# Kernel tuning notes

Measured on AMD Instinct MI355X. Metric: run time of the kernel, lower is better.

The kernel has to match this reference:

```python
import jax, jax.numpy as jnp
import numpy as np

M, P, B = 64, 256, 4096  # blocks per row/col, block size, batch


def setup_inputs() -> dict:
    key = jax.random.key(0)
    ks = jax.random.split(key, 6)
    u = lambda k, shape: jax.random.uniform(k, shape, jnp.float32, -0.1, 0.1)
    return {
        "x": jax.random.normal(ks[0], (B, M * P), dtype=jnp.float32),
        "Wd": u(ks[1], (M, P, P)),      # diag blocks (nn.Linear weights)
        "Wu": u(ks[2], (M - 1, P, P)),  # upper off-diagonal blocks
        "Wl": u(ks[3], (M - 1, P, P)),  # lower off-diagonal blocks
        "Wtr": u(ks[4], (P, P)),        # top-right corner block (periodic)
        "Wbl": u(ks[5], (P, P)),        # bottom-left corner block (periodic)
    }


def reference(x, Wd, Wu, Wl, Wtr, Wbl):
    # BlockXDiag forward, diag_type='tri', periodic=True, transpose=False,
    # bias=False, activation=None (identity). nn.Linear: o = x @ W.T
    Bsz = x.shape[0]
    xb = x.reshape(Bsz, M, P)  # [B, M, P]
    # diagonal: result[:, i] = x_i @ Wd[i].T  -> batched over all M blocks
    out = jnp.einsum('bip,iqp->biq', xb, Wd)
    # upper band: result[:, i] += x_{i+1} @ Wu[i].T, i in [0, M-2]
    out = out.at[:, : M - 1].add(jnp.einsum('bip,iqp->biq', xb[:, 1:], Wu))
    # lower band: result[:, i] += x_{i-1} @ Wl[i-1].T, i in [1, M-1]
    out = out.at[:, 1:].add(jnp.einsum('bip,iqp->biq', xb[:, : M - 1], Wl))
    # periodic corners
    out = out.at[:, 0].add(xb[:, M - 1] @ Wtr.T)
    out = out.at[:, M - 1].add(xb[:, 0] @ Wbl.T)
    return out.reshape(Bsz, M * P)
```

## Files before the change

kernel.cpp:

```cpp
#include <hip/hip_runtime.h>


#define MB   64
#define PB   256
#define NPR  16384
#define BSZ  4096
#define BM   128
#define BN   128
#define BK   32
#define KTOT 768

typedef __bf16 bf16x8 __attribute__((ext_vector_type(8)));
typedef float  f32x4  __attribute__((ext_vector_type(4)));
typedef unsigned short u16x4 __attribute__((ext_vector_type(4)));
typedef unsigned short u16x8 __attribute__((ext_vector_type(8)));

__device__ __forceinline__ unsigned short f2bf(float f) {
    unsigned u = __float_as_uint(f);
    u += 0x7fffu + ((u >> 16) & 1u);
    return (unsigned short)(u >> 16);
}

__device__ __forceinline__ void gload_lds16(const void* g, void* l) {
    __builtin_amdgcn_global_load_lds(
        (const __attribute__((address_space(1))) void*)g,
        (__attribute__((address_space(3))) void*)l, 16, 0, 0);
}

__global__ __launch_bounds__(256)
void cvt_x(const float* __restrict__ in, __bf16* __restrict__ o, int n8) {
    int idx    = blockIdx.x * 256 + threadIdx.x;
    int stride = gridDim.x * 256;
    for (; idx < n8; idx += stride) {
        const float4* p = (const float4*)in + (size_t)idx * 2;
        float4 a = p[0], b = p[1];
        u16x8 r = { f2bf(a.x), f2bf(a.y), f2bf(a.z), f2bf(a.w),
                    f2bf(b.x), f2bf(b.y), f2bf(b.z), f2bf(b.w) };
        *((u16x8*)o + idx) = r;
    }
}

__global__ __launch_bounds__(256)
void cvt_w(const float* __restrict__ Wd, const float* __restrict__ Wu,
           const float* __restrict__ Wl, const float* __restrict__ Wtr,
           const float* __restrict__ Wbl, __bf16* __restrict__ wcat) {
    const int i = blockIdx.y;
    const int c = blockIdx.z;
    const float* src;
    if      (c == 0) src = (i == 0)      ? Wtr : Wl + (size_t)(i - 1) * (PB * PB);
    else if (c == 1) src = Wd + (size_t)i * (PB * PB);
    else             src = (i == MB - 1) ? Wbl : Wu + (size_t)i * (PB * PB);

    const int off = (blockIdx.x * 256 + threadIdx.x) * 8;
    const float4* p = (const float4*)(src + off);
    float4 a = p[0], b = p[1];
    u16x8 r = { f2bf(a.x), f2bf(a.y), f2bf(a.z), f2bf(a.w),
                f2bf(b.x), f2bf(b.y), f2bf(b.z), f2bf(b.w) };
    *(u16x8*)(wcat + (size_t)(i * 3 + c) * (PB * PB) + off) = r;
}

__global__ __launch_bounds__(256, 4)
void bxd_bf16(const __bf16* __restrict__ xb, const __bf16* __restrict__ wcat,
              float* __restrict__ out)
{
    __shared__ __bf16 sA[BM * BK];
    __shared__ __bf16 sB[BN * BK];

    const int i  = blockIdx.x >> 1;
    const int nt = blockIdx.x & 1;
    const int mt = blockIdx.y;

    const int t    = threadIdx.x;
    const int lane = t & 63;
    const int wave = t >> 6;
    const int wm   = wave & 1;
    const int wn   = wave >> 1;
    const int quad = lane >> 4;
    const int l16  = lane & 15;

    const int jblk[3] = { (i + MB - 1) & (MB - 1), i, (i + 1) & (MB - 1) };

    const int row0 = t >> 2;
    const int kc   = (t & 3) * 8;

    f32x4 acc[4][4];
    #pragma unroll
    for (int a = 0; a < 4; ++a)
        #pragma unroll
        for (int b = 0; b < 4; ++b)
            acc[a][b] = (f32x4){0.f, 0.f, 0.f, 0.f};

    for (int kt = 0; kt < KTOT / BK; ++kt) {
        const int c  = kt >> 3;
        const int kb = kt & 7;

        const __bf16* aBase = xb + (size_t)(mt * BM) * NPR + jblk[c] * PB + kb * BK;
        const __bf16* bBase = wcat + (size_t)(i * 3 + c) * (PB * PB)
                                   + (size_t)(nt * BN) * PB + kb * BK;

        __syncthreads();
        #pragma unroll
        for (int p = 0; p < 2; ++p) {
            const int r = row0 + p * 64;
            gload_lds16(aBase + (size_t)r * NPR + kc, &sA[(t + p * 256) * 8]);
            gload_lds16(bBase + (size_t)r * PB  + kc, &sB[(t + p * 256) * 8]);
        }
        __syncthreads();

        bf16x8 afrag[4], bfrag[4];
        #pragma unroll
        for (int mi = 0; mi < 4; ++mi)
            afrag[mi] = *(const bf16x8*)&sA[(wm * 64 + mi * 16 + l16) * BK + quad * 8];
        #pragma unroll
        for (int ni = 0; ni < 4; ++ni)
            bfrag[ni] = *(const bf16x8*)&sB[(wn * 64 + ni * 16 + l16) * BK + quad * 8];

        #pragma unroll
        for (int mi = 0; mi < 4; ++mi)
            #pragma unroll
            for (int ni = 0; ni < 4; ++ni)
                acc[mi][ni] = __builtin_amdgcn_mfma_f32_16x16x32_bf16(
                    afrag[mi], bfrag[ni], acc[mi][ni], 0, 0, 0);
    }

    const int colb = i * PB + nt * BN + wn * 64;
    #pragma unroll
    for (int mi = 0; mi < 4; ++mi) {
        #pragma unroll
        for (int ni = 0; ni < 4; ++ni) {
            #pragma unroll
            for (int r = 0; r < 4; ++r) {
                const int row = mt * BM + wm * 64 + mi * 16 + quad * 4 + r;
                out[(size_t)row * NPR + colb + ni * 16 + l16] = acc[mi][ni][r];
            }
        }
    }
}

__global__ __launch_bounds__(256, 2)
void bxd_kernel(const float* __restrict__ x,
                const float* __restrict__ Wd,
                const float* __restrict__ Wu,
                const float* __restrict__ Wl,
                const float* __restrict__ Wtr,
                const float* __restrict__ Wbl,
                float* __restrict__ out)
{
    __shared__ unsigned short sA[BM * BK];
    __shared__ unsigned short sB[BN * BK];

    const int i  = blockIdx.x >> 1;
    const int nt = blockIdx.x & 1;
    const int mt = blockIdx.y;

    const int t    = threadIdx.x;
    const int lane = t & 63;
    const int wave = t >> 6;
    const int wm   = wave & 1;
    const int wn   = wave >> 1;
    const int quad = lane >> 4;
    const int l16  = lane & 15;

    const int srow = t >> 3;
    const int scol = (t & 7) * 4;

    const float* wptr[3];
    wptr[0] = (i == 0)      ? Wtr : (Wl + (size_t)(i - 1) * (PB * PB));
    wptr[1] = Wd + (size_t)i * (PB * PB);
    wptr[2] = (i == MB - 1) ? Wbl : (Wu + (size_t)i * (PB * PB));
    const int jblk[3] = { (i + MB - 1) & (MB - 1), i, (i + 1) & (MB - 1) };

    f32x4 acc[4][4];
    #pragma unroll
    for (int a = 0; a < 4; ++a)
        #pragma unroll
        for (int b = 0; b < 4; ++b)
            acc[a][b] = (f32x4){0.f, 0.f, 0.f, 0.f};

    for (int kt = 0; kt < KTOT / BK; ++kt) {
        const int c  = kt >> 3;
        const int kb = kt & 7;

        const float* aSrc = x + (size_t)(mt * BM + srow) * NPR
                              + jblk[c] * PB + kb * BK + scol;
        const float* bSrc = wptr[c] + (size_t)(nt * BN + srow) * PB
                              + kb * BK + scol;

        float4 av[4], bv[4];
        #pragma unroll
        for (int p = 0; p < 4; ++p) {
            av[p] = *(const float4*)(aSrc + (size_t)p * 32 * NPR);
            bv[p] = *(const float4*)(bSrc + (size_t)p * 32 * PB);
        }

        __syncthreads();
        #pragma unroll
        for (int p = 0; p < 4; ++p) {
            u16x4 ra = { f2bf(av[p].x), f2bf(av[p].y), f2bf(av[p].z), f2bf(av[p].w) };
            *(u16x4*)&sA[(srow + p * 32) * BK + scol] = ra;
            u16x4 rb = { f2bf(bv[p].x), f2bf(bv[p].y), f2bf(bv[p].z), f2bf(bv[p].w) };
            *(u16x4*)&sB[(srow + p * 32) * BK + scol] = rb;
        }
        __syncthreads();

        bf16x8 afrag[4], bfrag[4];
        #pragma unroll
        for (int mi = 0; mi < 4; ++mi)
            afrag[mi] = *(const bf16x8*)&sA[(wm * 64 + mi * 16 + l16) * BK + quad * 8];
        #pragma unroll
        for (int ni = 0; ni < 4; ++ni)
            bfrag[ni] = *(const bf16x8*)&sB[(wn * 64 + ni * 16 + l16) * BK + quad * 8];

        #pragma unroll
        for (int mi = 0; mi < 4; ++mi)
            #pragma unroll
            for (int ni = 0; ni < 4; ++ni)
                acc[mi][ni] = __builtin_amdgcn_mfma_f32_16x16x32_bf16(
                    afrag[mi], bfrag[ni], acc[mi][ni], 0, 0, 0);
    }

    const int colb = i * PB + nt * BN + wn * 64;
    #pragma unroll
    for (int mi = 0; mi < 4; ++mi) {
        #pragma unroll
        for (int ni = 0; ni < 4; ++ni) {
            #pragma unroll
            for (int r = 0; r < 4; ++r) {
                const int row = mt * BM + wm * 64 + mi * 16 + quad * 4 + r;
                out[(size_t)row * NPR + colb + ni * 16 + l16] = acc[mi][ni][r];
            }
        }
    }
}

extern "C" void kernel_launch(void* const* d_in, const int* in_sizes, int n_in,
                              void* d_out, int out_size, void* d_ws, size_t ws_size,
                              hipStream_t stream) {
    const float* x   = (const float*)d_in[0];
    const float* Wd  = (const float*)d_in[1];
    const float* Wu  = (const float*)d_in[2];
    const float* Wl  = (const float*)d_in[3];
    const float* Wtr = (const float*)d_in[4];
    const float* Wbl = (const float*)d_in[5];
    float* out = (float*)d_out;

    const size_t xbytes = (size_t)BSZ * NPR * sizeof(__bf16);
    const size_t wbytes = (size_t)MB * 3 * PB * PB * sizeof(__bf16);

    if (ws_size >= xbytes + wbytes) {
        __bf16* xbuf = (__bf16*)d_ws;
        __bf16* wcat = (__bf16*)((char*)d_ws + xbytes);
        hipLaunchKernelGGL(cvt_x, dim3(2048), dim3(256), 0, stream,
                           x, xbuf, (int)((size_t)BSZ * NPR / 8));
        hipLaunchKernelGGL(cvt_w, dim3(32, 64, 3), dim3(256), 0, stream,
                           Wd, Wu, Wl, Wtr, Wbl, wcat);
        hipLaunchKernelGGL(bxd_bf16, dim3(MB * 2, BSZ / BM), dim3(256), 0, stream,
                           xbuf, wcat, out);
    } else {
        dim3 grid(MB * 2, BSZ / BM, 1);
        dim3 block(256, 1, 1);
        hipLaunchKernelGGL(bxd_kernel, grid, block, 0, stream,
                           x, Wd, Wu, Wl, Wtr, Wbl, out);
    }
}
```

Measured before the change: 697.0 us.

## Enlarge bf16 GEMM tiles, double-buffer LDS with swizzle, remap block order

The bf16 kernel moves to 256x256x64 tiles with 512 threads and double-buffered LDS. The next K tile is loaded with global_load_lds while MFMAs run on the current one, and only one barrier is needed per iteration. LDS columns are XOR-swizzled to avoid bank conflicts, blocks are remapped so neighbouring workgroups share weight blocks, and s_setprio raises priority around the MFMA bursts. The larger tile increases register pressure (128 accumulator floats per thread) and uses 128KB of LDS per block, which may limit occupancy.

```diff
diff --git a/kernel.cpp b/kernel.cpp
--- a/kernel.cpp
+++ b/kernel.cpp
@@ -5,9 +5,10 @@
 #define PB   256
 #define NPR  16384
 #define BSZ  4096
-#define BM   128
-#define BN   128
-#define BK   32
+#define BM   256
+#define BN   256
+#define BK   64
+#define KTILES 12
 #define KTOT 768
 
 typedef __bf16 bf16x8 __attribute__((ext_vector_type(8)));
@@ -59,16 +60,17 @@
     *(u16x8*)(wcat + (size_t)(i * 3 + c) * (PB * PB) + off) = r;
 }
 
-__global__ __launch_bounds__(256, 4)
+__global__ __launch_bounds__(512, 2)
 void bxd_bf16(const __bf16* __restrict__ xb, const __bf16* __restrict__ wcat,
               float* __restrict__ out)
 {
-    __shared__ __bf16 sA[BM * BK];
-    __shared__ __bf16 sB[BN * BK];
-
-    const int i  = blockIdx.x >> 1;
-    const int nt = blockIdx.x & 1;
-    const int mt = blockIdx.y;
+    __shared__ __bf16 sA[2][BM * BK];
+    __shared__ __bf16 sB[2][BN * BK];
+
+    const int bid  = blockIdx.x;
+    const int slot = bid >> 3;
+    const int i    = (bid & 7) * 8 + (slot >> 4);
+    const int mt   = slot & 15;
 
     const int t    = threadIdx.x;
     const int lane = t & 63;
@@ -80,57 +82,75 @@
 
     const int jblk[3] = { (i + MB - 1) & (MB - 1), i, (i + 1) & (MB - 1) };
 
-    const int row0 = t >> 2;
-    const int kc   = (t & 3) * 8;
-
-    f32x4 acc[4][4];
-    #pragma unroll
-    for (int a = 0; a < 4; ++a)
+    const int rowS   = t >> 3;
+    const int srcoff = (((t & 7) ^ (rowS & 7))) * 8;
+
+    const int swz   = l16 & 7;
+    const int colE0 = ((quad)     ^ swz) * 8;
+    const int colE1 = ((4 + quad) ^ swz) * 8;
+    const int arow  = wm * 128 + l16;
+    const int brow  = wn * 64  + l16;
+
+    f32x4 acc[8][4];
+    #pragma unroll
+    for (int a = 0; a < 8; ++a)
         #pragma unroll
         for (int b = 0; b < 4; ++b)
             acc[a][b] = (f32x4){0.f, 0.f, 0.f, 0.f};
 
-    for (int kt = 0; kt < KTOT / BK; ++kt) {
-        const int c  = kt >> 3;
-        const int kb = kt & 7;
-
-        const __bf16* aBase = xb + (size_t)(mt * BM) * NPR + jblk[c] * PB + kb * BK;
-        const __bf16* bBase = wcat + (size_t)(i * 3 + c) * (PB * PB)
-                                   + (size_t)(nt * BN) * PB + kb * BK;
+    auto stage = [&](int b, int kt) {
+        const int c  = kt >> 2;
+        const int kb = kt & 3;
+        const __bf16* aB = xb + (size_t)(mt * BM) * NPR + jblk[c] * PB + kb * BK;
+        const __bf16* bB = wcat + (size_t)(i * 3 + c) * (PB * PB) + kb * BK;
+        #pragma unroll
+        for (int p = 0; p < 4; ++p) {
+            const int r = rowS + p * 64;
+            gload_lds16(aB + (size_t)r * NPR + srcoff, &sA[b][(t + p * 512) * 8]);
+            gload_lds16(bB + (size_t)r * PB  + srcoff, &sB[b][(t + p * 512) * 8]);
+        }
+    };
+
+    stage(0, 0);
+    __syncthreads();
+
+    int buf = 0;
+    for (int kt = 0; kt < KTILES; ++kt) {
+        if (kt + 1 < KTILES) stage(buf ^ 1, kt + 1);
+
+        #pragma unroll
+        for (int kh = 0; kh < 2; ++kh) {
+            const int colE = kh ? colE1 : colE0;
+            bf16x8 af[8], bfr[4];
+            #pragma unroll
+            for (int mi = 0; mi < 8; ++mi)
+                af[mi] = *(const bf16x8*)&sA[buf][(arow + mi * 16) * BK + colE];
+            #pragma unroll
+            for (int ni = 0; ni < 4; ++ni)
+                bfr[ni] = *(const bf16x8*)&sB[buf][(brow + ni * 16) * BK + colE];
+
+            __builtin_amdgcn_s_setprio(1);
+            #pragma unroll
+            for (int mi = 0; mi < 8; ++mi)
+                #pragma unroll
+                for (int ni = 0; ni < 4; ++ni)
+                    acc[mi][ni] = __builtin_amdgcn_mfma_f32_16x16x32_bf16(
+                        af[mi], bfr[ni], acc[mi][ni], 0, 0, 0);
+            __builtin_amdgcn_s_setprio(0);
+        }
 
         __syncthreads();
-        #pragma unroll
-        for (int p = 0; p < 2; ++p) {
-            const int r = row0 + p * 64;
-            gload_lds16(aBase + (size_t)r * NPR + kc, &sA[(t + p * 256) * 8]);
-            gload_lds16(bBase + (size_t)r * PB  + kc, &sB[(t + p * 256) * 8]);
-        }
-        __syncthreads();
-
-        bf16x8 afrag[4], bfrag[4];
-        #pragma unroll
-        for (int mi = 0; mi < 4; ++mi)
-            afrag[mi] = *(const bf16x8*)&sA[(wm * 64 + mi * 16 + l16) * BK + quad * 8];
-        #pragma unroll
-        for (int ni = 0; ni < 4; ++ni)
-            bfrag[ni] = *(const bf16x8*)&sB[(wn * 64 + ni * 16 + l16) * BK + quad * 8];
-
-        #pragma unroll
-        for (int mi = 0; mi < 4; ++mi)
-            #pragma unroll
-            for (int ni = 0; ni < 4; ++ni)
-                acc[mi][ni] = __builtin_amdgcn_mfma_f32_16x16x32_bf16(
-                    afrag[mi], bfrag[ni], acc[mi][ni], 0, 0, 0);
-    }
-
-    const int colb = i * PB + nt * BN + wn * 64;
-    #pragma unroll
-    for (int mi = 0; mi < 4; ++mi) {
+        buf ^= 1;
+    }
+
+    const int colb = i * PB + wn * 64;
+    #pragma unroll
+    for (int mi = 0; mi < 8; ++mi) {
         #pragma unroll
         for (int ni = 0; ni < 4; ++ni) {
             #pragma unroll
             for (int r = 0; r < 4; ++r) {
-                const int row = mt * BM + wm * 64 + mi * 16 + quad * 4 + r;
+                const int row = mt * BM + wm * 128 + mi * 16 + quad * 4 + r;
                 out[(size_t)row * NPR + colb + ni * 16 + l16] = acc[mi][ni][r];
             }
         }
@@ -146,8 +166,8 @@
                 const float* __restrict__ Wbl,
                 float* __restrict__ out)
 {
-    __shared__ unsigned short sA[BM * BK];
-    __shared__ unsigned short sB[BN * BK];
+    __shared__ unsigned short sA[128 * 32];
+    __shared__ unsigned short sB[128 * 32];
 
     const int i  = blockIdx.x >> 1;
     const int nt = blockIdx.x & 1;
@@ -177,14 +197,14 @@
         for (int b = 0; b < 4; ++b)
             acc[a][b] = (f32x4){0.f, 0.f, 0.f, 0.f};
 
-    for (int kt = 0; kt < KTOT / BK; ++kt) {
+    for (int kt = 0; kt < 24; ++kt) {
         const int c  = kt >> 3;
         const int kb = kt & 7;
 
-        const float* aSrc = x + (size_t)(mt * BM + srow) * NPR
-                              + jblk[c] * PB + kb * BK + scol;
-        const float* bSrc = wptr[c] + (size_t)(nt * BN + srow) * PB
-                              + kb * BK + scol;
+        const float* aSrc = x + (size_t)(mt * 128 + srow) * NPR
+                              + jblk[c] * PB + kb * 32 + scol;
+        const float* bSrc = wptr[c] + (size_t)(nt * 128 + srow) * PB
+                              + kb * 32 + scol;
 
         float4 av[4], bv[4];
         #pragma unroll
@@ -197,19 +217,19 @@
         #pragma unroll
         for (int p = 0; p < 4; ++p) {
             u16x4 ra = { f2bf(av[p].x), f2bf(av[p].y), f2bf(av[p].z), f2bf(av[p].w) };
-            *(u16x4*)&sA[(srow + p * 32) * BK + scol] = ra;
+            *(u16x4*)&sA[(srow + p * 32) * 32 + scol] = ra;
             u16x4 rb = { f2bf(bv[p].x), f2bf(bv[p].y), f2bf(bv[p].z), f2bf(bv[p].w) };
-            *(u16x4*)&sB[(srow + p * 32) * BK + scol] = rb;
+            *(u16x4*)&sB[(srow + p * 32) * 32 + scol] = rb;
         }
         __syncthreads();
 
         bf16x8 afrag[4], bfrag[4];
         #pragma unroll
         for (int mi = 0; mi < 4; ++mi)
-            afrag[mi] = *(const bf16x8*)&sA[(wm * 64 + mi * 16 + l16) * BK + quad * 8];
+            afrag[mi] = *(const bf16x8*)&sA[(wm * 64 + mi * 16 + l16) * 32 + quad * 8];
         #pragma unroll
         for (int ni = 0; ni < 4; ++ni)
-            bfrag[ni] = *(const bf16x8*)&sB[(wn * 64 + ni * 16 + l16) * BK + quad * 8];
+            bfrag[ni] = *(const bf16x8*)&sB[(wn * 64 + ni * 16 + l16) * 32 + quad * 8];
 
         #pragma unroll
         for (int mi = 0; mi < 4; ++mi)
@@ -219,14 +239,14 @@
                     afrag[mi], bfrag[ni], acc[mi][ni], 0, 0, 0);
     }
 
-    const int colb = i * PB + nt * BN + wn * 64;
+    const int colb = i * PB + nt * 128 + wn * 64;
     #pragma unroll
     for (int mi = 0; mi < 4; ++mi) {
         #pragma unroll
         for (int ni = 0; ni < 4; ++ni) {
             #pragma unroll
             for (int r = 0; r < 4; ++r) {
-                const int row = mt * BM + wm * 64 + mi * 16 + quad * 4 + r;
+                const int row = mt * 128 + wm * 64 + mi * 16 + quad * 4 + r;
                 out[(size_t)row * NPR + colb + ni * 16 + l16] = acc[mi][ni][r];
             }
         }
@@ -254,10 +274,10 @@
                            x, xbuf, (int)((size_t)BSZ * NPR / 8));
         hipLaunchKernelGGL(cvt_w, dim3(32, 64, 3), dim3(256), 0, stream,
                            Wd, Wu, Wl, Wtr, Wbl, wcat);
-        hipLaunchKernelGGL(bxd_bf16, dim3(MB * 2, BSZ / BM), dim3(256), 0, stream,
+        hipLaunchKernelGGL(bxd_bf16, dim3((MB) * (BSZ / BM)), dim3(512), 0, stream,
                            xbuf, wcat, out);
     } else {
-        dim3 grid(MB * 2, BSZ / BM, 1);
+        dim3 grid(MB * 2, BSZ / 128, 1);
         dim3 block(256, 1, 1);
         hipLaunchKernelGGL(bxd_kernel, grid, block, 0, stream,
                            x, Wd, Wu, Wl, Wtr, Wbl, out);
```

Measured after the change: 658.8 us. 1.06x faster.
